# Optimization experiments

Hardware: AMD Instinct MI355X
Metric: run time of the kernel (lower is better)

Reference implementation:

```python
import jax, jax.numpy as jnp
import numpy as np

B, D, H, W_ = 2, 256, 64, 64


def setup_inputs() -> dict:
    key = jax.random.key(0)
    k1, k2 = jax.random.split(key)
    x = jax.random.normal(k1, (B, D, H, W_), dtype=jnp.float32)
    W = jax.random.normal(k2, (3 * D, D), dtype=jnp.float32) * 0.02  # 1x1 conv weight [out,in]
    b = jnp.zeros((3 * D,), dtype=jnp.float32)
    return {"x": x, "W": W, "b": b}


def reference(x, W, b):
    Bs, d, h, w = x.shape
    N = h * w
    sqrtV = d ** 0.25  # sqrt(sqrt(d)); q,k each divided -> qk^T / sqrt(d)
    # 1x1 conv == per-pixel linear over channels
    qkv = jnp.einsum('bchw,oc->bohw', x, W) + b[None, :, None, None]
    q, k, v = jnp.split(qkv, 3, axis=1)
    q = q.reshape(Bs, d, N).transpose(0, 2, 1) / sqrtV  # [B,N,d]
    k = k.reshape(Bs, d, N).transpose(0, 2, 1) / sqrtV
    v = v.reshape(Bs, d, N).transpose(0, 2, 1)
    # Sinkhorn (eps=1, max_iter=1, uniform marginals 1/N), log domain.
    # cost C = -q k^T  =>  -C = q k^T (softmax-style logits)
    negC = jnp.einsum('bnd,bmd->bnm', q, k)  # [B,N,N]
    logm = jnp.log(1.0 / N + 1e-8).astype(x.dtype)
    u = logm - jax.nn.logsumexp(negC, axis=-1)            # [B,N] row update
    vpot = logm - jax.nn.logsumexp(negC + u[..., None], axis=-2)  # [B,N] col update
    pi = jnp.exp(negC + u[..., None] + vpot[:, None, :])  # transport plan = attn
    out = jnp.einsum('bnm,bmd->bnd', pi, v)               # [B,N,d]
    return out.transpose(0, 2, 1).reshape(Bs, d, h, w)
```

## Files before the change

kernel.cpp:

```cpp
#include <hip/hip_runtime.h>
#include <hip/hip_bf16.h>
#include <math.h>

typedef __bf16 bf16;
typedef __bf16 bf16x8 __attribute__((ext_vector_type(8)));
typedef __bf16 bf16x4 __attribute__((ext_vector_type(4)));
typedef float floatx4 __attribute__((ext_vector_type(4)));

typedef const __attribute__((address_space(1))) void* gas_t;
typedef __attribute__((address_space(3))) void* las_t;

#define NPIX 4096
#define DCH 256

#define OFF_XB   ((size_t)0)
#define OFF_WB   ((size_t)4194304)
#define OFF_Q    ((size_t)4587520)
#define OFF_K    ((size_t)8781824)
#define OFF_V    ((size_t)12976128)
#define OFF_E    ((size_t)17170432)
#define OFF_VPP  ((size_t)84279296)
#define OFF_RP   ((size_t)88473600)
#define OFF_CP   ((size_t)89522176)
#define OFF_PART ((size_t)90570752)

__device__ __forceinline__ void stage_tile(const bf16* __restrict__ g0, size_t rstride,
                                           bf16* lds, int t) {
  const int wbase = (t >> 6) << 6;
#pragma unroll
  for (int i = 0; i < 4; i++) {
    int slot = i * 256 + t;
    int row = slot >> 3, seg = slot & 7;
    const bf16* g = g0 + (size_t)row * rstride + ((seg ^ (row & 7)) << 3);
    bf16* l = lds + (size_t)(i * 256 + wbase) * 8;
    __builtin_amdgcn_global_load_lds((gas_t)g, (las_t)l, 16, 0, 0);
  }
}

__global__ __launch_bounds__(256) void prep(
    const float* __restrict__ x, const float* __restrict__ W,
    bf16* __restrict__ xb, bf16* __restrict__ wb)
{
  const int t = threadIdx.x;
  if (blockIdx.y == 4) {
    int gid = (blockIdx.z * 64 + blockIdx.x) * 256 + t;
    for (int i = gid; i < 49152; i += 32768) {
      float4 v = *(const float4*)(W + (size_t)i * 4);
      bf16x4 pk = { (bf16)v.x, (bf16)v.y, (bf16)v.z, (bf16)v.w };
      *(bf16x4*)(wb + (size_t)i * 4) = pk;
    }
    return;
  }
  __shared__ float ts[64][65];
  const int b = blockIdx.z, n0 = blockIdx.x * 64, c0 = blockIdx.y * 64;
  const float* xp = x + ((size_t)b * DCH + c0) * NPIX + n0;
  for (int i = 0; i < 4; i++) {
    int slot = t + i * 256;
    int c = slot >> 4, nq = (slot & 15) * 4;
    float4 v = *(const float4*)(xp + (size_t)c * NPIX + nq);
    ts[c][nq + 0] = v.x; ts[c][nq + 1] = v.y; ts[c][nq + 2] = v.z; ts[c][nq + 3] = v.w;
  }
  __syncthreads();
  for (int i = 0; i < 2; i++) {
    int slot = t + i * 256;
    int n = slot >> 3, cq = (slot & 7) * 8;
    bf16x8 pk;
    for (int j = 0; j < 8; j++) pk[j] = (bf16)ts[cq + j][n];
    *(bf16x8*)(xb + ((size_t)b * NPIX + n0 + n) * DCH + c0 + cq) = pk;
  }
}

__global__ __launch_bounds__(256) void conv_mfma(
    const bf16* __restrict__ xb, const bf16* __restrict__ wb,
    const float* __restrict__ bias,
    bf16* __restrict__ qb, bf16* __restrict__ kb, bf16* __restrict__ vb)
{
  __shared__ bf16 at[128 * 64];
  __shared__ bf16 bt[128 * 64];
  __shared__ float bs[128];
  const int t  = threadIdx.x;
  const int n0 = blockIdx.x * 128;
  const int o0 = blockIdx.y * 128;
  if (t < 128) bs[t] = bias[o0 + t];
  const int lane = t & 63, wave = t >> 6;
  const int wm = wave >> 1, wn = wave & 1;
  const int l15 = lane & 15, quad = lane >> 4;
  const int l7 = l15 & 7;

  floatx4 acc[4][4];
  for (int i=0;i<4;i++) for (int j=0;j<4;j++) for (int r=0;r<4;r++) acc[i][j][r] = 0.f;

  for (int k0 = 0; k0 < DCH; k0 += 64) {
    stage_tile(wb + (size_t)o0 * DCH + k0, DCH, at, t);
    stage_tile(xb + (size_t)n0 * DCH + k0, DCH, bt, t);
    __syncthreads();
    for (int kk = 0; kk < 2; kk++) {
      bf16x8 af[4], bfr[4];
      int sw = ((kk * 4 + quad) ^ l7) * 8;
      for (int f = 0; f < 4; f++)
        af[f]  = *(const bf16x8*)&at[(wm*64 + f*16 + l15)*64 + sw];
      for (int f = 0; f < 4; f++)
        bfr[f] = *(const bf16x8*)&bt[(wn*64 + f*16 + l15)*64 + sw];
      for (int fm = 0; fm < 4; fm++)
        for (int fn = 0; fn < 4; fn++)
          acc[fm][fn] = __builtin_amdgcn_mfma_f32_16x16x32_bf16(af[fm], bfr[fn], acc[fm][fn], 0, 0, 0);
    }
    __syncthreads();
  }

  const float scale = (o0 < 512) ? 0.25f : 1.0f;
  bf16* dst; int od;
  if (o0 < 256)      { dst = qb; od = o0; }
  else if (o0 < 512) { dst = kb; od = o0 - 256; }
  else               { dst = vb; od = o0 - 512; }

  for (int fm = 0; fm < 4; fm++)
    for (int fn = 0; fn < 4; fn++) {
      int o_l = wm*64 + fm*16 + quad*4;
      int n_g = n0 + wn*64 + fn*16 + l15;
      bf16x4 pk;
      for (int r = 0; r < 4; r++)
        pk[r] = (bf16)((acc[fm][fn][r] + bs[o_l + r]) * scale);
      *(bf16x4*)(dst + (size_t)n_g * DCH + od + o_l) = pk;
    }
}

__global__ __launch_bounds__(256) void pass_a(
    const bf16* __restrict__ qb, const bf16* __restrict__ kb,
    bf16* __restrict__ E, float* __restrict__ rowpartG)
{
  __shared__ bf16 kt[128 * 64];
  __shared__ bf16 qt[128 * 64];
  __shared__ float rowpart[128];
  const int b = blockIdx.z;
  qb += (size_t)b * NPIX * DCH;
  kb += (size_t)b * NPIX * DCH;
  E  += (size_t)b * NPIX * NPIX;
  float* rp = rowpartG + ((size_t)b * 32 + blockIdx.x) * NPIX;
  const int t  = threadIdx.x;
  const int m0 = blockIdx.x * 128;
  const int n0 = blockIdx.y * 128;
  const int lane = t & 63, wave = t >> 6;
  const int wm = wave >> 1, wn = wave & 1;
  const int l15 = lane & 15, quad = lane >> 4;
  const int l7 = l15 & 7;

  floatx4 acc[4][4];
  for (int i=0;i<4;i++) for (int j=0;j<4;j++) for (int r=0;r<4;r++) acc[i][j][r] = 0.f;

  for (int k0 = 0; k0 < DCH; k0 += 64) {
    stage_tile(kb + (size_t)m0 * DCH + k0, DCH, kt, t);
    stage_tile(qb + (size_t)n0 * DCH + k0, DCH, qt, t);
    __syncthreads();
    for (int kk = 0; kk < 2; kk++) {
      bf16x8 af[4], bfr[4];
      int sw = ((kk * 4 + quad) ^ l7) * 8;
      for (int f = 0; f < 4; f++)
        af[f]  = *(const bf16x8*)&kt[(wm*64 + f*16 + l15)*64 + sw];
      for (int f = 0; f < 4; f++)
        bfr[f] = *(const bf16x8*)&qt[(wn*64 + f*16 + l15)*64 + sw];
      for (int fm = 0; fm < 4; fm++)
        for (int fn = 0; fn < 4; fn++)
          acc[fm][fn] = __builtin_amdgcn_mfma_f32_16x16x32_bf16(af[fm], bfr[fn], acc[fm][fn], 0, 0, 0);
    }
    __syncthreads();
  }

  if (t < 128) rowpart[t] = 0.f;
  __syncthreads();

  float rsum[4] = {0.f, 0.f, 0.f, 0.f};
  for (int fm = 0; fm < 4; fm++)
    for (int fn = 0; fn < 4; fn++) {
      int n_g = n0 + wn*64 + fn*16 + l15;
      int m_g = m0 + wm*64 + fm*16 + quad*4;
      bf16x4 pk;
      float s = 0.f;
      for (int r = 0; r < 4; r++) {
        float e = __expf(acc[fm][fn][r]);
        pk[r] = (bf16)e;
        s += e;
      }
      *(bf16x4*)(E + (size_t)n_g * NPIX + m_g) = pk;
      rsum[fn] += s;
    }
  for (int fn = 0; fn < 4; fn++) {
    float s = rsum[fn];
    s += __shfl_xor(s, 16);
    s += __shfl_xor(s, 32);
    if (quad == 0) atomicAdd(&rowpart[wn*64 + fn*16 + l15], s);
  }
  __syncthreads();
  if (t < 128) rp[n0 + t] = rowpart[t];
}

__global__ __launch_bounds__(256) void col_pass(
    const bf16* __restrict__ E, const float* __restrict__ rowpartG,
    float* __restrict__ colpartG, float logm)
{
  __shared__ float eus[128];
  const int b = blockIdx.z;
  E += (size_t)b * NPIX * NPIX;
  const float* rp = rowpartG + (size_t)b * 32 * NPIX;
  float* cp = colpartG + ((size_t)b * 32 + blockIdx.y) * NPIX;
  const int t = threadIdx.x;
  const int col = blockIdx.x * 1024 + t * 4;
  const int nbase = blockIdx.y * 128;
  if (t < 128) {
    float s = 0.f;
    for (int mi = 0; mi < 32; mi++) s += rp[(size_t)mi * NPIX + nbase + t];
    eus[t] = __expf(logm - __logf(s));
  }
  __syncthreads();
  float a0 = 0.f, a1 = 0.f, a2 = 0.f, a3 = 0.f;
  for (int r = 0; r < 128; r++) {
    float eu = eus[r];
    bf16x4 ev = *(const bf16x4*)(E + (size_t)(nbase + r) * NPIX + col);
    a0 += eu * (float)ev[0];
    a1 += eu * (float)ev[1];
    a2 += eu * (float)ev[2];
    a3 += eu * (float)ev[3];
  }
  float4 o = {a0, a1, a2, a3};
  *(float4*)(cp + col) = o;
}

__global__ __launch_bounds__(256) void vpp_kernel(
    const bf16* __restrict__ vb, const float* __restrict__ colpartG,
    bf16* __restrict__ vppT, float logm)
{
  __shared__ float ts[64][65];
  __shared__ float ef[64];
  const int b = blockIdx.z;
  vb += (size_t)b * NPIX * DCH;
  const float* cp = colpartG + (size_t)b * 32 * NPIX;
  vppT += (size_t)b * DCH * NPIX;
  const int t = threadIdx.x;
  const int m0 = blockIdx.x * 64, d0 = blockIdx.y * 64;
  if (t < 64) {
    float s = 0.f;
    for (int g = 0; g < 32; g++) s += cp[(size_t)g * NPIX + m0 + t];
    ef[t] = __expf(logm - __logf(s));
  }
  __syncthreads();
  for (int i = 0; i < 2; i++) {
    int slot = t + i * 256;
    int m = slot >> 3, dq = (slot & 7) * 8;
    bf16x8 v = *(const bf16x8*)(vb + (size_t)(m0 + m) * DCH + d0 + dq);
    float s = ef[m];
    for (int j = 0; j < 8; j++) ts[dq + j][m] = s * (float)v[j];
  }
  __syncthreads();
  for (int i = 0; i < 2; i++) {
    int slot = t + i * 256;
    int d = slot >> 3, mq = (slot & 7) * 8;
    bf16x8 pk;
    for (int j = 0; j < 8; j++) pk[j] = (bf16)ts[d][mq + j];
    *(bf16x8*)(vppT + (size_t)(d0 + d) * NPIX + m0 + mq) = pk;
  }
}

__global__ __launch_bounds__(256) void pass_c(
    const bf16* __restrict__ E, const bf16* __restrict__ vppT,
    const float* __restrict__ rowpartG, bf16* __restrict__ part, float logm)
{
  __shared__ bf16 et[128 * 64];
  __shared__ bf16 vt[128 * 64];
  __shared__ float eus[128];
  const int z = blockIdx.z;
  const int b = z >> 2, kc = z & 3;
  E += (size_t)b * NPIX * NPIX;
  vppT += (size_t)b * DCH * NPIX;
  const float* rp = rowpartG + (size_t)b * 32 * NPIX;
  part += (size_t)(b * 4 + kc) * DCH * NPIX;
  const int t  = threadIdx.x;
  const int n0 = blockIdx.x * 128;
  const int d0 = blockIdx.y * 128;
  const int mstart = kc * 1024;
  if (t < 128) {
    float s = 0.f;
    for (int mi = 0; mi < 32; mi++) s += rp[(size_t)mi * NPIX + n0 + t];
    eus[t] = __expf(logm - __logf(s));
  }
  const int lane = t & 63, wave = t >> 6;
  const int wn = wave >> 1, wd = wave & 1;
  const int l15 = lane & 15, quad = lane >> 4;
  const int l7 = l15 & 7;

  floatx4 acc[4][4];
  for (int i=0;i<4;i++) for (int j=0;j<4;j++) for (int r=0;r<4;r++) acc[i][j][r] = 0.f;
  __syncthreads();

  for (int k0 = mstart; k0 < mstart + 1024; k0 += 64) {
    stage_tile(E + (size_t)n0 * NPIX + k0, NPIX, et, t);
    stage_tile(vppT + (size_t)d0 * NPIX + k0, NPIX, vt, t);
    __syncthreads();
    for (int kk = 0; kk < 2; kk++) {
      bf16x8 af[4], bfr[4];
      int sw = ((kk * 4 + quad) ^ l7) * 8;
      for (int f = 0; f < 4; f++)
        af[f]  = *(const bf16x8*)&et[(wn*64 + f*16 + l15)*64 + sw];
      for (int f = 0; f < 4; f++)
        bfr[f] = *(const bf16x8*)&vt[(wd*64 + f*16 + l15)*64 + sw];
      for (int fn = 0; fn < 4; fn++)
        for (int fd = 0; fd < 4; fd++)
          acc[fn][fd] = __builtin_amdgcn_mfma_f32_16x16x32_bf16(af[fn], bfr[fd], acc[fn][fd], 0, 0, 0);
    }
    __syncthreads();
  }

  for (int fn = 0; fn < 4; fn++)
    for (int fd = 0; fd < 4; fd++) {
      int d_g = d0 + wd*64 + fd*16 + l15;
      int n_l = wn*64 + fn*16 + quad*4;
      bf16x4 o;
      o[0] = (bf16)(acc[fn][fd][0] * eus[n_l + 0]);
      o[1] = (bf16)(acc[fn][fd][1] * eus[n_l + 1]);
      o[2] = (bf16)(acc[fn][fd][2] * eus[n_l + 2]);
      o[3] = (bf16)(acc[fn][fd][3] * eus[n_l + 3]);
      *(bf16x4*)(part + (size_t)d_g * NPIX + n0 + n_l) = o;
    }
}

__global__ __launch_bounds__(256) void reduce_k(
    const bf16* __restrict__ part, float* __restrict__ outp)
{
  size_t i4 = ((size_t)blockIdx.x * 256 + threadIdx.x) * 4;
  size_t b = i4 >> 20;
  size_t off = i4 & (size_t)1048575;
  const bf16* p = part + b * 4 * (size_t)1048576 + off;
  bf16x4 a = *(const bf16x4*)(p);
  bf16x4 bq = *(const bf16x4*)(p + (size_t)1048576);
  bf16x4 c = *(const bf16x4*)(p + (size_t)2097152);
  bf16x4 d = *(const bf16x4*)(p + (size_t)3145728);
  float4 s = { (float)a[0]+(float)bq[0]+(float)c[0]+(float)d[0],
               (float)a[1]+(float)bq[1]+(float)c[1]+(float)d[1],
               (float)a[2]+(float)bq[2]+(float)c[2]+(float)d[2],
               (float)a[3]+(float)bq[3]+(float)c[3]+(float)d[3] };
  *(float4*)(outp + i4) = s;
}

extern "C" void kernel_launch(void* const* d_in, const int* in_sizes, int n_in,
                              void* d_out, int out_size, void* d_ws, size_t ws_size,
                              hipStream_t stream) {
  (void)in_sizes; (void)n_in; (void)out_size; (void)ws_size;
  const float* x    = (const float*)d_in[0];
  const float* Wm   = (const float*)d_in[1];
  const float* bias = (const float*)d_in[2];
  float* outp = (float*)d_out;
  char* ws = (char*)d_ws;

  bf16*  xb   = (bf16*)(ws + OFF_XB);
  bf16*  wb   = (bf16*)(ws + OFF_WB);
  bf16*  qb   = (bf16*)(ws + OFF_Q);
  bf16*  kb   = (bf16*)(ws + OFF_K);
  bf16*  vb   = (bf16*)(ws + OFF_V);
  bf16*  E    = (bf16*)(ws + OFF_E);
  bf16*  vppT = (bf16*)(ws + OFF_VPP);
  float* rp   = (float*)(ws + OFF_RP);
  float* cp   = (float*)(ws + OFF_CP);
  bf16*  part = (bf16*)(ws + OFF_PART);

  const float logm = logf(1.0f / 4096.0f + 1e-8f);

  prep<<<dim3(64, 5, 2), 256, 0, stream>>>(x, Wm, xb, wb);
  conv_mfma<<<dim3(64, 6), 256, 0, stream>>>(xb, wb, bias, qb, kb, vb);

  pass_a<<<dim3(32, 32, 2), 256, 0, stream>>>(qb, kb, E, rp);
  col_pass<<<dim3(4, 32, 2), 256, 0, stream>>>(E, rp, cp, logm);
  vpp_kernel<<<dim3(64, 4, 2), 256, 0, stream>>>(vb, cp, vppT, logm);
  pass_c<<<dim3(32, 2, 8), 256, 0, stream>>>(E, vppT, rp, part, logm);
  reduce_k<<<2048, 256, 0, stream>>>(part, outp);
}
```

Baseline: 156.5 us.

## Double-buffer LDS tiles with async prefetch in conv, pass_a and pass_c GEMMs

Converts the three MFMA GEMM kernels to double-buffered LDS staging. The next K-slice is issued with global_load_lds before computing on the current one, and explicit vmcnt waits plus raw s_barrier replace __syncthreads. This is meant to overlap global-to-LDS transfer with MFMA work. In exchange LDS use doubles per block, which may lower occupancy, and correctness now depends on the hand-written vmcnt counts.

```diff
diff --git a/kernel.cpp b/kernel.cpp
--- a/kernel.cpp
+++ b/kernel.cpp
@@ -37,6 +37,7 @@
   }
 }
 
+
 __global__ __launch_bounds__(256) void prep(
     const float* __restrict__ x, const float* __restrict__ W,
     bf16* __restrict__ xb, bf16* __restrict__ wb)
@@ -75,8 +76,8 @@
     const float* __restrict__ bias,
     bf16* __restrict__ qb, bf16* __restrict__ kb, bf16* __restrict__ vb)
 {
-  __shared__ bf16 at[128 * 64];
-  __shared__ bf16 bt[128 * 64];
+  __shared__ bf16 at[2][128 * 64];
+  __shared__ bf16 bt[2][128 * 64];
   __shared__ float bs[128];
   const int t  = threadIdx.x;
   const int n0 = blockIdx.x * 128;
@@ -87,25 +88,37 @@
   const int l15 = lane & 15, quad = lane >> 4;
   const int l7 = l15 & 7;
 
+  stage_tile(wb + (size_t)o0 * DCH, DCH, at[0], t);
+  stage_tile(xb + (size_t)n0 * DCH, DCH, bt[0], t);
+
   floatx4 acc[4][4];
   for (int i=0;i<4;i++) for (int j=0;j<4;j++) for (int r=0;r<4;r++) acc[i][j][r] = 0.f;
 
-  for (int k0 = 0; k0 < DCH; k0 += 64) {
-    stage_tile(wb + (size_t)o0 * DCH + k0, DCH, at, t);
-    stage_tile(xb + (size_t)n0 * DCH + k0, DCH, bt, t);
-    __syncthreads();
+#pragma unroll
+  for (int kidx = 0; kidx < 4; kidx++) {
+    const int cur = kidx & 1;
+    if (kidx < 3) {
+      stage_tile(wb + (size_t)o0 * DCH + (kidx + 1) * 64, DCH, at[cur ^ 1], t);
+      stage_tile(xb + (size_t)n0 * DCH + (kidx + 1) * 64, DCH, bt[cur ^ 1], t);
+      asm volatile("s_waitcnt vmcnt(8)" ::: "memory");
+    } else {
+      asm volatile("s_waitcnt vmcnt(0)" ::: "memory");
+    }
+    __builtin_amdgcn_s_barrier();
+    asm volatile("" ::: "memory");
     for (int kk = 0; kk < 2; kk++) {
       bf16x8 af[4], bfr[4];
       int sw = ((kk * 4 + quad) ^ l7) * 8;
       for (int f = 0; f < 4; f++)
-        af[f]  = *(const bf16x8*)&at[(wm*64 + f*16 + l15)*64 + sw];
-      for (int f = 0; f < 4; f++)
-        bfr[f] = *(const bf16x8*)&bt[(wn*64 + f*16 + l15)*64 + sw];
+        af[f]  = *(const bf16x8*)&at[cur][(wm*64 + f*16 + l15)*64 + sw];
+      for (int f = 0; f < 4; f++)
+        bfr[f] = *(const bf16x8*)&bt[cur][(wn*64 + f*16 + l15)*64 + sw];
       for (int fm = 0; fm < 4; fm++)
         for (int fn = 0; fn < 4; fn++)
           acc[fm][fn] = __builtin_amdgcn_mfma_f32_16x16x32_bf16(af[fm], bfr[fn], acc[fm][fn], 0, 0, 0);
     }
-    __syncthreads();
+    asm volatile("" ::: "memory");
+    __builtin_amdgcn_s_barrier();
   }
 
   const float scale = (o0 < 512) ? 0.25f : 1.0f;
@@ -129,8 +142,8 @@
     const bf16* __restrict__ qb, const bf16* __restrict__ kb,
     bf16* __restrict__ E, float* __restrict__ rowpartG)
 {
-  __shared__ bf16 kt[128 * 64];
-  __shared__ bf16 qt[128 * 64];
+  __shared__ bf16 kt[2][128 * 64];
+  __shared__ bf16 qt[2][128 * 64];
   __shared__ float rowpart[128];
   const int b = blockIdx.z;
   qb += (size_t)b * NPIX * DCH;
@@ -145,25 +158,37 @@
   const int l15 = lane & 15, quad = lane >> 4;
   const int l7 = l15 & 7;
 
+  stage_tile(kb + (size_t)m0 * DCH, DCH, kt[0], t);
+  stage_tile(qb + (size_t)n0 * DCH, DCH, qt[0], t);
+
   floatx4 acc[4][4];
   for (int i=0;i<4;i++) for (int j=0;j<4;j++) for (int r=0;r<4;r++) acc[i][j][r] = 0.f;
 
-  for (int k0 = 0; k0 < DCH; k0 += 64) {
-    stage_tile(kb + (size_t)m0 * DCH + k0, DCH, kt, t);
-    stage_tile(qb + (size_t)n0 * DCH + k0, DCH, qt, t);
-    __syncthreads();
+#pragma unroll
+  for (int kidx = 0; kidx < 4; kidx++) {
+    const int cur = kidx & 1;
+    if (kidx < 3) {
+      stage_tile(kb + (size_t)m0 * DCH + (kidx + 1) * 64, DCH, kt[cur ^ 1], t);
+      stage_tile(qb + (size_t)n0 * DCH + (kidx + 1) * 64, DCH, qt[cur ^ 1], t);
+      asm volatile("s_waitcnt vmcnt(8)" ::: "memory");
+    } else {
+      asm volatile("s_waitcnt vmcnt(0)" ::: "memory");
+    }
+    __builtin_amdgcn_s_barrier();
+    asm volatile("" ::: "memory");
     for (int kk = 0; kk < 2; kk++) {
       bf16x8 af[4], bfr[4];
       int sw = ((kk * 4 + quad) ^ l7) * 8;
       for (int f = 0; f < 4; f++)
-        af[f]  = *(const bf16x8*)&kt[(wm*64 + f*16 + l15)*64 + sw];
-      for (int f = 0; f < 4; f++)
-        bfr[f] = *(const bf16x8*)&qt[(wn*64 + f*16 + l15)*64 + sw];
+        af[f]  = *(const bf16x8*)&kt[cur][(wm*64 + f*16 + l15)*64 + sw];
+      for (int f = 0; f < 4; f++)
+        bfr[f] = *(const bf16x8*)&qt[cur][(wn*64 + f*16 + l15)*64 + sw];
       for (int fm = 0; fm < 4; fm++)
         for (int fn = 0; fn < 4; fn++)
           acc[fm][fn] = __builtin_amdgcn_mfma_f32_16x16x32_bf16(af[fm], bfr[fn], acc[fm][fn], 0, 0, 0);
     }
-    __syncthreads();
+    asm volatile("" ::: "memory");
+    __builtin_amdgcn_s_barrier();
   }
 
   if (t < 128) rowpart[t] = 0.f;
@@ -264,8 +289,8 @@
     const bf16* __restrict__ E, const bf16* __restrict__ vppT,
     const float* __restrict__ rowpartG, bf16* __restrict__ part, float logm)
 {
-  __shared__ bf16 et[128 * 64];
-  __shared__ bf16 vt[128 * 64];
+  __shared__ bf16 et[2][128 * 64];
+  __shared__ bf16 vt[2][128 * 64];
   __shared__ float eus[128];
   const int z = blockIdx.z;
   const int b = z >> 2, kc = z & 3;
@@ -291,22 +316,35 @@
   for (int i=0;i<4;i++) for (int j=0;j<4;j++) for (int r=0;r<4;r++) acc[i][j][r] = 0.f;
   __syncthreads();
 
-  for (int k0 = mstart; k0 < mstart + 1024; k0 += 64) {
-    stage_tile(E + (size_t)n0 * NPIX + k0, NPIX, et, t);
-    stage_tile(vppT + (size_t)d0 * NPIX + k0, NPIX, vt, t);
-    __syncthreads();
+  stage_tile(E + (size_t)n0 * NPIX + mstart, NPIX, et[0], t);
+  stage_tile(vppT + (size_t)d0 * NPIX + mstart, NPIX, vt[0], t);
+
+#pragma unroll 4
+  for (int kidx = 0; kidx < 16; kidx++) {
+    const int cur = kidx & 1;
+    if (kidx < 15) {
+      const int kn = mstart + (kidx + 1) * 64;
+      stage_tile(E + (size_t)n0 * NPIX + kn, NPIX, et[cur ^ 1], t);
+      stage_tile(vppT + (size_t)d0 * NPIX + kn, NPIX, vt[cur ^ 1], t);
+      asm volatile("s_waitcnt vmcnt(8)" ::: "memory");
+    } else {
+      asm volatile("s_waitcnt vmcnt(0)" ::: "memory");
+    }
+    __builtin_amdgcn_s_barrier();
+    asm volatile("" ::: "memory");
     for (int kk = 0; kk < 2; kk++) {
       bf16x8 af[4], bfr[4];
       int sw = ((kk * 4 + quad) ^ l7) * 8;
       for (int f = 0; f < 4; f++)
-        af[f]  = *(const bf16x8*)&et[(wn*64 + f*16 + l15)*64 + sw];
-      for (int f = 0; f < 4; f++)
-        bfr[f] = *(const bf16x8*)&vt[(wd*64 + f*16 + l15)*64 + sw];
+        af[f]  = *(const bf16x8*)&et[cur][(wn*64 + f*16 + l15)*64 + sw];
+      for (int f = 0; f < 4; f++)
+        bfr[f] = *(const bf16x8*)&vt[cur][(wd*64 + f*16 + l15)*64 + sw];
       for (int fn = 0; fn < 4; fn++)
         for (int fd = 0; fd < 4; fd++)
           acc[fn][fd] = __builtin_amdgcn_mfma_f32_16x16x32_bf16(af[fn], bfr[fd], acc[fn][fd], 0, 0, 0);
     }
-    __syncthreads();
+    asm volatile("" ::: "memory");
+    __builtin_amdgcn_s_barrier();
   }
 
   for (int fn = 0; fn < 4; fn++)
```

New measurement: 157.3 us. About the same (+0.5%).
